# Optimization experiments

Measured on AMD Instinct MI355X. Metric: run time of the kernel, lower is better.

## Reference

```python
import jax, jax.numpy as jnp
import numpy as np

B, Z, H, T = 256, 512, 1024, 512   # batch, z_size, hidden (conductor==decoder), num_tokens
L, N = 16, 16                      # num_levels, notes_per_bar


def setup_inputs() -> dict:
    key = jax.random.key(0)
    ks = jax.random.split(key, 16)
    s = 0.05  # weight init scale
    rn = lambda k, shp, sc=1.0: sc * jax.random.normal(k, shp, dtype=jnp.float32)
    return {
        "z": rn(ks[0], (B, L * N, 1, Z)),
        "dec_h0": rn(ks[1], (L, B, H)),
        "dec_c0": rn(ks[2], (L, B, H)),
        # linear_in (computed but unused by the original forward)
        "lin_in_W": rn(ks[3], (Z, Z), s), "lin_in_b": rn(ks[4], (Z,), s),
        # conductor LSTM (input Z -> hidden H), PyTorch gate order i,f,g,o
        "cond_Wih": rn(ks[5], (4 * H, Z), s), "cond_Whh": rn(ks[6], (4 * H, H), s),
        "cond_bih": rn(ks[7], (4 * H,), s), "cond_bhh": rn(ks[8], (4 * H,), s),
        # decoder LSTM (input T+H -> hidden H)
        "dec_Wih": rn(ks[9], (4 * H, T + H), s), "dec_Whh": rn(ks[10], (4 * H, H), s),
        "dec_bih": rn(ks[11], (4 * H,), s), "dec_bhh": rn(ks[12], (4 * H,), s),
        # output projection
        "out_W": rn(ks[13], (T, H), s), "out_b": rn(ks[14], (T,), s),
    }


def _lstm_cell(x, h, c, Wih, Whh, b):
    gates = x @ Wih.T + h @ Whh.T + b            # [B, 4H]
    i, f, g, o = jnp.split(gates, 4, axis=-1)
    c = jax.nn.sigmoid(f) * c + jax.nn.sigmoid(i) * jnp.tanh(g)
    h = jax.nn.sigmoid(o) * jnp.tanh(c)
    return h, c


def reference(z, dec_h0, dec_c0, lin_in_W, lin_in_b,
              cond_Wih, cond_Whh, cond_bih, cond_bhh,
              dec_Wih, dec_Whh, dec_bih, dec_bhh, out_W, out_b):
    Bsz = z.shape[0]
    Tt = out_b.shape[0]
    Hh = cond_Whh.shape[1]

    _unused = z @ lin_in_W.T + lin_in_b  # linear_in output is discarded in the source

    cond_b = cond_bih + cond_bhh
    dec_b = dec_bih + dec_bhh

    # conductor consumes z[:, L*level, 0, :] for each level
    z_lv = jnp.transpose(z[:, jnp.arange(L) * L, 0, :], (1, 0, 2))  # [L, B, Z]

    def level_step(carry, xs):
        ch, cc = carry
        zl, dh, dc = xs
        ch, cc = _lstm_cell(zl, ch, cc, cond_Wih, cond_Whh, cond_b)
        emb = ch  # [B, H], fixed conductor embedding for this bar

        def note_step(c2, _):
            note, dh2, dc2 = c2
            inp = jnp.concatenate([emb, note], axis=-1)  # [B, H+T]
            dh2, dc2 = _lstm_cell(inp, dh2, dc2, dec_Wih, dec_Whh, dec_b)
            out = jax.nn.sigmoid(dh2 @ out_W.T + out_b)  # [B, T]
            return (out, dh2, dc2), out

        note0 = jnp.zeros((Bsz, Tt), dtype=z.dtype)
        _, outs = jax.lax.scan(note_step, (note0, dh, dc), None, length=N)  # [N, B, T]
        return (ch, cc), outs

    h0 = jnp.zeros((Bsz, Hh), dtype=z.dtype)
    _, all_outs = jax.lax.scan(level_step, (h0, h0), (z_lv, dec_h0, dec_c0))  # [L, N, B, T]
    notes = jnp.transpose(all_outs, (2, 0, 1, 3)).reshape(Bsz, L * N, Tt)
    return notes
```

## Files before the change

### kernel.cpp

```cpp
#include <hip/hip_runtime.h>

typedef __bf16 bf16;
typedef __attribute__((ext_vector_type(8))) __bf16 bf16x8;
typedef __attribute__((ext_vector_type(4))) float f32x4;
typedef __attribute__((ext_vector_type(4))) unsigned short u16x4;

__device__ __forceinline__ void gload_lds16(const void* g, void* l) {
  __builtin_amdgcn_global_load_lds(
      (const __attribute__((address_space(1))) void*)g,
      (__attribute__((address_space(3))) void*)l, 16, 0, 0);
}

__device__ __forceinline__ float sigmoidf_(float x) { return 1.0f / (1.0f + expf(-x)); }

__device__ __forceinline__ float bf2f(unsigned short u) {
  union { unsigned int i; float f; } v;
  v.i = ((unsigned int)u) << 16;
  return v.f;
}
__device__ __forceinline__ unsigned short f2bfbits(float x) {
  union { bf16 b; unsigned short u; } v;
  v.b = (bf16)x;
  return v.u;
}

#define SB() __builtin_amdgcn_sched_barrier(0)
#define BAR()                          \
  do {                                 \
    SB();                              \
    __builtin_amdgcn_s_barrier();      \
    SB();                              \
  } while (0)

#define MFMA16(a, b, c) __builtin_amdgcn_mfma_f32_16x16x32_bf16(a, b, c, 0, 0, 0)

template<int MODE>
__global__ __launch_bounds__(512, 2)
void gemm8(const bf16* __restrict__ A, int lda,
           const bf16* __restrict__ Bw, int K,
           bf16* __restrict__ Cb,
           const bf16* __restrict__ X, const float* __restrict__ bias,
           float* __restrict__ cst, bf16* __restrict__ hout, int ldh) {
  extern __shared__ __align__(16) char smem_raw[];
  bf16* lsA = (bf16*)smem_raw;
  bf16* lsB = lsA + 2 * 16384;

  const int tid = threadIdx.x;
  const int lane = tid & 63;
  const int wave = tid >> 6;
  const int wm = wave >> 2, wn = wave & 3;

  const int bid = blockIdx.x;
  const int wgid = (bid & 7) * 32 + (bid >> 3);
  const int m0 = (wgid >> 4) * 256, n0 = (wgid & 15) * 256;

  const int nkt = K >> 6;

  const int srow = tid >> 3;
  const int csw = ((tid & 7) * 8) ^ ((srow & 7) << 3);
  const bf16* gA = A + (size_t)m0 * lda + csw;
  const bf16* gB = Bw + (size_t)n0 * K + csw;

  auto stageA = [&](int kt) {
    bf16* d = lsA + (kt & 1) * 16384 + tid * 8;
    const bf16* s = gA + (size_t)srow * lda + (size_t)kt * 64;
    gload_lds16(s, d);
    gload_lds16(s + (size_t)64 * lda, d + 4096);
    gload_lds16(s + (size_t)128 * lda, d + 8192);
    gload_lds16(s + (size_t)192 * lda, d + 12288);
  };
  auto stageB = [&](int kt) {
    bf16* d = lsB + (kt & 1) * 16384 + tid * 8;
    const bf16* s = gB + (size_t)srow * K + (size_t)kt * 64;
    gload_lds16(s, d);
    gload_lds16(s + (size_t)64 * K, d + 4096);
    gload_lds16(s + (size_t)128 * K, d + 8192);
    gload_lds16(s + (size_t)192 * K, d + 12288);
  };

  const int c0 = ((lane >> 4) * 8) ^ ((lane & 7) << 3);
  const int c1 = c0 ^ 32;
  const int abase = (wm * 128 + (lane & 15)) * 64;
  const int bbase = (wn * 64 + (lane & 15)) * 64;

  f32x4 acc[8][4] = {};

  stageA(0); stageB(0);
  if (nkt > 1) stageB(1);
  if (nkt > 1) asm volatile("s_waitcnt vmcnt(4)" ::: "memory");
  else         asm volatile("s_waitcnt vmcnt(0)" ::: "memory");
  BAR();

  for (int u = 0; u < nkt; ++u) {
    const int c = u & 1;
    const bf16* pA = lsA + c * 16384;
    const bf16* pB = lsB + c * 16384;
    bf16x8 avA[4], avB[4], avC[4], avD[4], bvA[4], bvB[4];

    if (u + 1 < nkt) stageA(u + 1);
#pragma unroll
    for (int f = 0; f < 4; ++f) avA[f] = *(const bf16x8*)&pA[abase + f * 1024 + c0];
#pragma unroll
    for (int g = 0; g < 4; ++g) bvA[g] = *(const bf16x8*)&pB[bbase + g * 1024 + c0];
#pragma unroll
    for (int f = 0; f < 4; ++f) avB[f] = *(const bf16x8*)&pA[abase + (f + 4) * 1024 + c0];
    BAR();
    __builtin_amdgcn_s_setprio(1);
#pragma unroll
    for (int f = 0; f < 4; ++f)
#pragma unroll
      for (int g = 0; g < 4; ++g)
        acc[f][g] = MFMA16(avA[f], bvA[g], acc[f][g]);
    __builtin_amdgcn_s_setprio(0);
    BAR();

#pragma unroll
    for (int f = 0; f < 4; ++f) avC[f] = *(const bf16x8*)&pA[abase + f * 1024 + c1];
#pragma unroll
    for (int g = 0; g < 4; ++g) bvB[g] = *(const bf16x8*)&pB[bbase + g * 1024 + c1];
    __builtin_amdgcn_s_setprio(1);
#pragma unroll
    for (int f = 0; f < 4; ++f)
#pragma unroll
      for (int g = 0; g < 4; ++g)
        acc[f + 4][g] = MFMA16(avB[f], bvA[g], acc[f + 4][g]);
    __builtin_amdgcn_s_setprio(0);
    BAR();

#pragma unroll
    for (int f = 0; f < 4; ++f) avD[f] = *(const bf16x8*)&pA[abase + (f + 4) * 1024 + c1];
    __builtin_amdgcn_s_setprio(1);
#pragma unroll
    for (int f = 0; f < 4; ++f)
#pragma unroll
      for (int g = 0; g < 4; ++g)
        acc[f][g] = MFMA16(avC[f], bvB[g], acc[f][g]);
    __builtin_amdgcn_s_setprio(0);
    BAR();

    if (u + 2 < nkt) stageB(u + 2);
    SB();
    __builtin_amdgcn_s_setprio(1);
#pragma unroll
    for (int f = 0; f < 4; ++f)
#pragma unroll
      for (int g = 0; g < 4; ++g)
        acc[f + 4][g] = MFMA16(avD[f], bvB[g], acc[f + 4][g]);
    __builtin_amdgcn_s_setprio(0);
    if (u + 2 < nkt)      asm volatile("s_waitcnt vmcnt(4)" ::: "memory");
    else if (u + 1 < nkt) asm volatile("s_waitcnt vmcnt(0)" ::: "memory");
    BAR();
  }

  const int jj = lane & 15;
  const int rb = m0 + wm * 128 + ((lane >> 4) << 2);
  const int q = (n0 >> 6) + wn;
  if constexpr (MODE == 0) {
#pragma unroll
    for (int f = 0; f < 8; ++f)
#pragma unroll
      for (int r = 0; r < 4; ++r) {
        u16x4 pk;
        pk[0] = f2bfbits(acc[f][0][r]);
        pk[1] = f2bfbits(acc[f][1][r]);
        pk[2] = f2bfbits(acc[f][2][r]);
        pk[3] = f2bfbits(acc[f][3][r]);
        *(u16x4*)&Cb[(size_t)(rb + f * 16 + r) * 4096 + q * 64 + jj * 4] = pk;
      }
  } else {
    const int j = q * 16 + jj;
    const f32x4 bq = *(const f32x4*)&bias[q * 64 + jj * 4];
#pragma unroll
    for (int f = 0; f < 8; ++f) {
#pragma unroll
      for (int r = 0; r < 4; ++r) {
        const int row = rb + f * 16 + r;
        const u16x4 xv = *(const u16x4*)&X[(size_t)row * 4096 + q * 64 + jj * 4];
        const float gi = acc[f][0][r] + bf2f(xv[0]) + bq[0];
        const float gf = acc[f][1][r] + bf2f(xv[1]) + bq[1];
        const float gg = acc[f][2][r] + bf2f(xv[2]) + bq[2];
        const float go = acc[f][3][r] + bf2f(xv[3]) + bq[3];
        const size_t ci = (size_t)row * 1024 + j;
        const float cn = sigmoidf_(gf) * cst[ci] + sigmoidf_(gi) * tanhf(gg);
        cst[ci] = cn;
        hout[(size_t)row * ldh + j] = (bf16)(sigmoidf_(go) * tanhf(cn));
      }
    }
  }
}

template<int BM, int BN, int WM, int WN, int MODE>
__global__ __launch_bounds__(WM * WN * 64)
void gemm_bt(const bf16* __restrict__ A, int lda,
             const bf16* __restrict__ Bw, int ldb,
             float* __restrict__ C, int ldc, int K,
             const float* __restrict__ outb, float* __restrict__ dout,
             bf16* __restrict__ anote, int nstep) {
  constexpr int BK = 64;
  constexpr int THREADS = WM * WN * 64;
  constexpr int SM = BM / WM, SN = BN / WN;
  constexpr int FM = SM / 16, FN = SN / 16;

  __shared__ __align__(16) bf16 lsA[BM * BK];
  __shared__ __align__(16) bf16 lsB[BN * BK];

  const int tid = threadIdx.x;
  const int lane = tid & 63;
  const int wave = tid >> 6;
  const int wm = wave / WN, wn = wave % WN;
  const int m0 = blockIdx.y * BM;
  const int n0 = blockIdx.x * BN;

  f32x4 acc[FM][FN] = {};

  const bf16* gA = A + (size_t)m0 * lda;
  const bf16* gB = Bw + (size_t)n0 * ldb;

  for (int k0 = 0; k0 < K; k0 += BK) {
#pragma unroll
    for (int i = 0; i < (BM * 8) / THREADS; ++i) {
      int idx = i * THREADS + tid;
      gload_lds16(gA + (size_t)(idx >> 3) * lda + k0 + (idx & 7) * 8, &lsA[idx * 8]);
    }
#pragma unroll
    for (int i = 0; i < (BN * 8) / THREADS; ++i) {
      int idx = i * THREADS + tid;
      gload_lds16(gB + (size_t)(idx >> 3) * ldb + k0 + (idx & 7) * 8, &lsB[idx * 8]);
    }
    __syncthreads();

#pragma unroll
    for (int kk = 0; kk < BK; kk += 32) {
      bf16x8 av[FM], bv[FN];
#pragma unroll
      for (int i = 0; i < FM; ++i)
        av[i] = *(const bf16x8*)&lsA[(wm * SM + i * 16 + (lane & 15)) * BK + kk + (lane >> 4) * 8];
#pragma unroll
      for (int j = 0; j < FN; ++j)
        bv[j] = *(const bf16x8*)&lsB[(wn * SN + j * 16 + (lane & 15)) * BK + kk + (lane >> 4) * 8];
#pragma unroll
      for (int i = 0; i < FM; ++i)
#pragma unroll
        for (int j = 0; j < FN; ++j)
          acc[i][j] = MFMA16(av[i], bv[j], acc[i][j]);
    }
    __syncthreads();
  }

#pragma unroll
  for (int i = 0; i < FM; ++i) {
#pragma unroll
    for (int j = 0; j < FN; ++j) {
      const int col = n0 + wn * SN + j * 16 + (lane & 15);
      const int rbase = m0 + wm * SM + i * 16 + ((lane >> 4) << 2);
#pragma unroll
      for (int r = 0; r < 4; ++r) {
        const int row = rbase + r;
        float v = acc[i][j][r];
        if constexpr (MODE == 0) {
          C[(size_t)row * ldc + col] = v;
        } else {
          v = sigmoidf_(v + outb[col]);
          const int l = row >> 8, b = row & 255;
          dout[((size_t)(b * 256 + l * 16 + nstep)) * 512 + col] = v;
          anote[(size_t)row * 1536 + col] = (bf16)v;
        }
      }
    }
  }
}

template<int BM, int BJ, int WM, int WJ>
__global__ __launch_bounds__(WM * WJ * 64, 2)
void gemm_cell(const bf16* __restrict__ A, int lda,
               const bf16* __restrict__ Bw,
               const bf16* __restrict__ X,
               const float* __restrict__ bias,
               float* __restrict__ cst,
               bf16* __restrict__ hout, int ldh, int K) {
  constexpr int BK = 64;
  constexpr int THREADS = WM * WJ * 64;
  constexpr int BN = BJ * 64;
  constexpr int SM = BM / WM;
  constexpr int TJ = BJ / WJ;
  constexpr int FM = SM / 16;

  __shared__ __align__(16) bf16 lsA[BM * BK];
  __shared__ __align__(16) bf16 lsB[BN * BK];

  const int tid = threadIdx.x;
  const int lane = tid & 63;
  const int wave = tid >> 6;
  const int wm = wave / WJ, wj = wave % WJ;
  const int m0 = blockIdx.y * BM;
  const int qb = blockIdx.x * BJ;

  f32x4 acc[FM][TJ][4] = {};

  const bf16* gA = A + (size_t)m0 * lda;
  const bf16* gB = Bw + (size_t)(qb * 64) * K;

  for (int k0 = 0; k0 < K; k0 += BK) {
#pragma unroll
    for (int i = 0; i < (BM * 8) / THREADS; ++i) {
      int idx = i * THREADS + tid;
      gload_lds16(gA + (size_t)(idx >> 3) * lda + k0 + (idx & 7) * 8, &lsA[idx * 8]);
    }
#pragma unroll
    for (int i = 0; i < (BN * 8) / THREADS; ++i) {
      int idx = i * THREADS + tid;
      gload_lds16(gB + (size_t)(idx >> 3) * K + k0 + (idx & 7) * 8, &lsB[idx * 8]);
    }
    __syncthreads();

#pragma unroll
    for (int kk = 0; kk < BK; kk += 32) {
      bf16x8 av[FM], bv[TJ][4];
#pragma unroll
      for (int i = 0; i < FM; ++i)
        av[i] = *(const bf16x8*)&lsA[(wm * SM + i * 16 + (lane & 15)) * BK + kk + (lane >> 4) * 8];
#pragma unroll
      for (int t = 0; t < TJ; ++t)
#pragma unroll
        for (int g = 0; g < 4; ++g)
          bv[t][g] = *(const bf16x8*)
              &lsB[((wj * TJ + t) * 64 + g * 16 + (lane & 15)) * BK + kk + (lane >> 4) * 8];
#pragma unroll
      for (int i = 0; i < FM; ++i)
#pragma unroll
        for (int t = 0; t < TJ; ++t)
#pragma unroll
          for (int g = 0; g < 4; ++g)
            acc[i][t][g] = MFMA16(av[i], bv[t][g], acc[i][t][g]);
    }
    __syncthreads();
  }

#pragma unroll
  for (int i = 0; i < FM; ++i) {
#pragma unroll
    for (int t = 0; t < TJ; ++t) {
      const int q = qb + wj * TJ + t;
      const int jj = lane & 15;
      const int j = q * 16 + jj;
      const int rbase = m0 + wm * SM + i * 16 + ((lane >> 4) << 2);
      const f32x4 bq = *(const f32x4*)&bias[q * 64 + jj * 4];
#pragma unroll
      for (int r = 0; r < 4; ++r) {
        const int row = rbase + r;
        const u16x4 xv = *(const u16x4*)&X[(size_t)row * 4096 + q * 64 + jj * 4];
        const float gi = acc[i][t][0][r] + bf2f(xv[0]) + bq[0];
        const float gf = acc[i][t][1][r] + bf2f(xv[1]) + bq[1];
        const float gg = acc[i][t][2][r] + bf2f(xv[2]) + bq[2];
        const float go = acc[i][t][3][r] + bf2f(xv[3]) + bq[3];
        const size_t ci = (size_t)row * 1024 + j;
        const float c = sigmoidf_(gf) * cst[ci] + sigmoidf_(gi) * tanhf(gg);
        cst[ci] = c;
        hout[(size_t)row * ldh + j] = (bf16)(sigmoidf_(go) * tanhf(c));
      }
    }
  }
}


__global__ void conv_f32_bf16(const float* __restrict__ src, bf16* __restrict__ dst, int n) {
  int idx = blockIdx.x * 256 + threadIdx.x;
  if (idx < n) dst[idx] = (bf16)src[idx];
}

__device__ __forceinline__ int p_src_row(int n) {
  int q = n >> 6, gate = (n >> 4) & 3, jj = n & 15;
  return gate * 1024 + q * 16 + jj;
}

__global__ void pack_w_dec(const float* __restrict__ wih, const float* __restrict__ whh,
                           bf16* __restrict__ dst) {
  int idx = blockIdx.x * 256 + threadIdx.x;
  int n = idx / 1536, c = idx - n * 1536;
  int r = p_src_row(n);
  float v = (c < 512) ? wih[(size_t)r * 1536 + 1024 + c] : whh[(size_t)r * 1024 + (c - 512)];
  dst[idx] = (bf16)v;
}

__global__ void pack_w_emb(const float* __restrict__ wih, bf16* __restrict__ dst) {
  int idx = blockIdx.x * 256 + threadIdx.x;
  int n = idx >> 10, c = idx & 1023;
  dst[idx] = (bf16)wih[(size_t)p_src_row(n) * 1536 + c];
}

__global__ void pack_w_perm(const float* __restrict__ src, bf16* __restrict__ dst, int Kw) {
  int idx = blockIdx.x * 256 + threadIdx.x;
  int n = idx / Kw, c = idx - n * Kw;
  dst[idx] = (bf16)src[(size_t)p_src_row(n) * Kw + c];
}

__global__ void pack_bias(const float* __restrict__ bih, const float* __restrict__ bhh,
                          float* __restrict__ dst) {
  int n = blockIdx.x * 256 + threadIdx.x;
  int q = n >> 6, jj = (n >> 2) & 15, g = n & 3;
  int r = g * 1024 + q * 16 + jj;
  dst[n] = bih[r] + bhh[r];
}

__global__ void pack_zb(const float* __restrict__ z, bf16* __restrict__ dst) {
  int idx = blockIdx.x * 256 + threadIdx.x;
  int m = idx >> 9, k = idx & 511;
  int l = m >> 8, b = m & 255;
  dst[idx] = (bf16)z[((size_t)b * 256 + 16 * l) * 512 + k];
}

__global__ void init_cond(float* __restrict__ cc, bf16* __restrict__ hz0) {
  int idx = blockIdx.x * 256 + threadIdx.x;
  cc[idx] = 0.f;
  hz0[idx] = (bf16)0.f;
}

__global__ void init_state(const float* __restrict__ h0, const float* __restrict__ c0,
                           bf16* __restrict__ Abuf, float* __restrict__ cdec) {
  int idx = blockIdx.x * 256 + threadIdx.x;
  int m = idx / 1536, c = idx - m * 1536;
  if (c < 512) {
    Abuf[idx] = (bf16)0.f;
  } else {
    int j = c - 512;
    size_t s = (size_t)m * 1024 + j;
    Abuf[idx] = (bf16)h0[s];
    cdec[s] = c0[s];
  }
}

extern "C" void kernel_launch(void* const* d_in, const int* in_sizes, int n_in,
                              void* d_out, int out_size, void* d_ws, size_t ws_size,
                              hipStream_t stream) {
  const float* z        = (const float*)d_in[0];
  const float* dec_h0   = (const float*)d_in[1];
  const float* dec_c0   = (const float*)d_in[2];
  const float* cond_Wih = (const float*)d_in[5];
  const float* cond_Whh = (const float*)d_in[6];
  const float* cond_bih = (const float*)d_in[7];
  const float* cond_bhh = (const float*)d_in[8];
  const float* dec_Wih  = (const float*)d_in[9];
  const float* dec_Whh  = (const float*)d_in[10];
  const float* dec_bih  = (const float*)d_in[11];
  const float* dec_bhh  = (const float*)d_in[12];
  const float* out_W    = (const float*)d_in[13];
  const float* out_b    = (const float*)d_in[14];
  float* out = (float*)d_out;

  char* ws = (char*)d_ws;
  size_t off = 0;
  auto alloc = [&](size_t bytes) {
    void* p = ws + off;
    off += (bytes + 255) & ~(size_t)255;
    return p;
  };
  bf16* E     = (bf16*)alloc(4096ull * 4096 * 2);
  bf16* Xz    = (bf16*)alloc(4096ull * 4096 * 2);
  float* cdec = (float*)alloc(4096ull * 1024 * 4);
  bf16* Abuf  = (bf16*)alloc(4096ull * 1536 * 2);
  bf16* Wd    = (bf16*)alloc(4096ull * 1536 * 2);
  bf16* We    = (bf16*)alloc(4096ull * 1024 * 2);
  bf16* Wcih  = (bf16*)alloc(4096ull * 512 * 2);
  bf16* Wchh  = (bf16*)alloc(4096ull * 1024 * 2);
  bf16* Wo    = (bf16*)alloc(512ull * 1024 * 2);
  float* cc   = (float*)alloc(256ull * 1024 * 4);
  bf16* emb   = (bf16*)alloc(4096ull * 1024 * 2);
  bf16* Zb    = (bf16*)alloc(4096ull * 512 * 2);
  bf16* hz0   = (bf16*)alloc(256ull * 1024 * 2);
  float* bdP  = (float*)alloc(4096ull * 4);
  float* bcP  = (float*)alloc(4096ull * 4);

  dim3 b256(256);

  hipFuncSetAttribute(reinterpret_cast<const void*>(&gemm8<0>),
                      hipFuncAttributeMaxDynamicSharedMemorySize, 131072);
  hipFuncSetAttribute(reinterpret_cast<const void*>(&gemm8<1>),
                      hipFuncAttributeMaxDynamicSharedMemorySize, 131072);

  pack_w_perm<<<4096 * 512 / 256, b256, 0, stream>>>(cond_Wih, Wcih, 512);
  pack_w_perm<<<4096 * 1024 / 256, b256, 0, stream>>>(cond_Whh, Wchh, 1024);
  conv_f32_bf16<<<(512 * 1024 + 255) / 256, b256, 0, stream>>>(out_W, Wo, 512 * 1024);
  pack_w_dec<<<4096 * 1536 / 256, b256, 0, stream>>>(dec_Wih, dec_Whh, Wd);
  pack_w_emb<<<4096 * 1024 / 256, b256, 0, stream>>>(dec_Wih, We);
  pack_bias<<<16, b256, 0, stream>>>(dec_bih, dec_bhh, bdP);
  pack_bias<<<16, b256, 0, stream>>>(cond_bih, cond_bhh, bcP);
  pack_zb<<<4096 * 512 / 256, b256, 0, stream>>>(z, Zb);
  init_cond<<<256 * 1024 / 256, b256, 0, stream>>>(cc, hz0);
  init_state<<<4096 * 1536 / 256, b256, 0, stream>>>(dec_h0, dec_c0, Abuf, cdec);

  gemm8<0><<<256, 512, 131072, stream>>>(Zb, 512, Wcih, 512, Xz,
                                         nullptr, nullptr, nullptr, nullptr, 0);

  for (int l = 0; l < 16; ++l) {
    const bf16* hprev = (l == 0) ? hz0 : (emb + (size_t)(l - 1) * 256 * 1024);
    gemm_cell<32, 2, 2, 2><<<dim3(32, 8), dim3(256), 0, stream>>>(
        hprev, 1024, Wchh, Xz + (size_t)l * 256 * 4096, bcP,
        cc, emb + (size_t)l * 256 * 1024, 1024, 1024);
  }

  gemm8<0><<<256, 512, 131072, stream>>>(emb, 1024, We, 1024, E,
                                         nullptr, nullptr, nullptr, nullptr, 0);

  for (int n = 0; n < 16; ++n) {
    gemm8<1><<<256, 512, 131072, stream>>>(Abuf, 1536, Wd, 1536, nullptr,
                                           E, bdP, cdec, Abuf + 512, 1536);
    gemm_bt<128, 64, 2, 2, 1><<<dim3(512 / 64, 4096 / 128), dim3(256), 0, stream>>>(
        Abuf + 512, 1536, Wo, 1024, nullptr, 0, 1024, out_b, out, Abuf, n);
  }
}
```

Before: 1.750 ms.

## Split GEMM tile staging into half-tiles interleaved across MFMA phases

Breaks the global-to-LDS staging of the A and B tiles into two 128-row halves and issues them at different points among the four MFMA phases of each k-step. The B prefetch schedule changes to one half two steps ahead and one half one step ahead, with adjusted vmcnt waits. Fragment loads are reordered to cut the number of live register vectors. The aim is to spread memory traffic more evenly and lower register pressure. The cost is more barriers and a more delicate double-buffer hazard ordering, where the LDS halves being overwritten must already be consumed.

```diff
diff --git a/kernel.cpp b/kernel.cpp
--- a/kernel.cpp
+++ b/kernel.cpp
@@ -61,21 +61,17 @@
   const bf16* gA = A + (size_t)m0 * lda + csw;
   const bf16* gB = Bw + (size_t)n0 * K + csw;
 
-  auto stageA = [&](int kt) {
-    bf16* d = lsA + (kt & 1) * 16384 + tid * 8;
-    const bf16* s = gA + (size_t)srow * lda + (size_t)kt * 64;
+  auto stageA = [&](int kt, int h) {
+    bf16* d = lsA + (kt & 1) * 16384 + h * 8192 + tid * 8;
+    const bf16* s = gA + (size_t)(h * 128 + srow) * lda + (size_t)kt * 64;
     gload_lds16(s, d);
     gload_lds16(s + (size_t)64 * lda, d + 4096);
-    gload_lds16(s + (size_t)128 * lda, d + 8192);
-    gload_lds16(s + (size_t)192 * lda, d + 12288);
   };
-  auto stageB = [&](int kt) {
-    bf16* d = lsB + (kt & 1) * 16384 + tid * 8;
-    const bf16* s = gB + (size_t)srow * K + (size_t)kt * 64;
+  auto stageB = [&](int kt, int h) {
+    bf16* d = lsB + (kt & 1) * 16384 + h * 8192 + tid * 8;
+    const bf16* s = gB + (size_t)(h * 128 + srow) * K + (size_t)kt * 64;
     gload_lds16(s, d);
     gload_lds16(s + (size_t)64 * K, d + 4096);
-    gload_lds16(s + (size_t)128 * K, d + 8192);
-    gload_lds16(s + (size_t)192 * K, d + 12288);
   };
 
   const int c0 = ((lane >> 4) * 8) ^ ((lane & 7) << 3);
@@ -85,71 +81,88 @@
 
   f32x4 acc[8][4] = {};
 
-  stageA(0); stageB(0);
-  if (nkt > 1) stageB(1);
-  if (nkt > 1) asm volatile("s_waitcnt vmcnt(4)" ::: "memory");
-  else         asm volatile("s_waitcnt vmcnt(0)" ::: "memory");
+  stageA(0, 0); stageA(0, 1); stageB(0, 0); stageB(0, 1);
+  if (nkt > 1) {
+    stageB(1, 0);
+    asm volatile("s_waitcnt vmcnt(2)" ::: "memory");
+  } else {
+    asm volatile("s_waitcnt vmcnt(0)" ::: "memory");
+  }
   BAR();
 
   for (int u = 0; u < nkt; ++u) {
-    const int c = u & 1;
-    const bf16* pA = lsA + c * 16384;
-    const bf16* pB = lsB + c * 16384;
-    bf16x8 avA[4], avB[4], avC[4], avD[4], bvA[4], bvB[4];
-
-    if (u + 1 < nkt) stageA(u + 1);
-#pragma unroll
-    for (int f = 0; f < 4; ++f) avA[f] = *(const bf16x8*)&pA[abase + f * 1024 + c0];
-#pragma unroll
-    for (int g = 0; g < 4; ++g) bvA[g] = *(const bf16x8*)&pB[bbase + g * 1024 + c0];
-#pragma unroll
-    for (int f = 0; f < 4; ++f) avB[f] = *(const bf16x8*)&pA[abase + (f + 4) * 1024 + c0];
+    const int cb = u & 1;
+    const bf16* pA = lsA + cb * 16384;
+    const bf16* pB = lsB + cb * 16384;
+    bf16x8 av[4], bv[4];
+
+#pragma unroll
+    for (int f = 0; f < 4; ++f) av[f] = *(const bf16x8*)&pA[abase + f * 1024 + c0];
+#pragma unroll
+    for (int g = 0; g < 4; ++g) bv[g] = *(const bf16x8*)&pB[bbase + g * 1024 + c0];
+    if (u + 1 < nkt) { stageA(u + 1, 0); stageB(u + 1, 1); }
     BAR();
     __builtin_amdgcn_s_setprio(1);
 #pragma unroll
     for (int f = 0; f < 4; ++f)
 #pragma unroll
       for (int g = 0; g < 4; ++g)
-        acc[f][g] = MFMA16(avA[f], bvA[g], acc[f][g]);
+        acc[f][g] = MFMA16(av[f], bv[g], acc[f][g]);
     __builtin_amdgcn_s_setprio(0);
     BAR();
 
-#pragma unroll
-    for (int f = 0; f < 4; ++f) avC[f] = *(const bf16x8*)&pA[abase + f * 1024 + c1];
-#pragma unroll
-    for (int g = 0; g < 4; ++g) bvB[g] = *(const bf16x8*)&pB[bbase + g * 1024 + c1];
+    {
+      bf16x8 a1[4];
+#pragma unroll
+      for (int f = 0; f < 4; ++f) a1[f] = *(const bf16x8*)&pA[abase + (f + 4) * 1024 + c0];
+      if (u + 1 < nkt) stageA(u + 1, 1);
+      BAR();
+      __builtin_amdgcn_s_setprio(1);
+#pragma unroll
+      for (int f = 0; f < 4; ++f)
+#pragma unroll
+        for (int g = 0; g < 4; ++g)
+          acc[f + 4][g] = MFMA16(a1[f], bv[g], acc[f + 4][g]);
+      __builtin_amdgcn_s_setprio(0);
+      BAR();
+    }
+
+#pragma unroll
+    for (int f = 0; f < 4; ++f) av[f] = *(const bf16x8*)&pA[abase + f * 1024 + c1];
+#pragma unroll
+    for (int g = 0; g < 4; ++g) bv[g] = *(const bf16x8*)&pB[bbase + g * 1024 + c1];
+    BAR();
     __builtin_amdgcn_s_setprio(1);
 #pragma unroll
     for (int f = 0; f < 4; ++f)
 #pragma unroll
       for (int g = 0; g < 4; ++g)
-        acc[f + 4][g] = MFMA16(avB[f], bvA[g], acc[f + 4][g]);
+        acc[f][g] = MFMA16(av[f], bv[g], acc[f][g]);
     __builtin_amdgcn_s_setprio(0);
     BAR();
 
-#pragma unroll
-    for (int f = 0; f < 4; ++f) avD[f] = *(const bf16x8*)&pA[abase + (f + 4) * 1024 + c1];
-    __builtin_amdgcn_s_setprio(1);
-#pragma unroll
-    for (int f = 0; f < 4; ++f)
-#pragma unroll
-      for (int g = 0; g < 4; ++g)
-        acc[f][g] = MFMA16(avC[f], bvB[g], acc[f][g]);
-    __builtin_amdgcn_s_setprio(0);
-    BAR();
-
-    if (u + 2 < nkt) stageB(u + 2);
-    SB();
-    __builtin_amdgcn_s_setprio(1);
-#pragma unroll
-    for (int f = 0; f < 4; ++f)
-#pragma unroll
-      for (int g = 0; g < 4; ++g)
-        acc[f + 4][g] = MFMA16(avD[f], bvB[g], acc[f + 4][g]);
-    __builtin_amdgcn_s_setprio(0);
-    if (u + 2 < nkt)      asm volatile("s_waitcnt vmcnt(4)" ::: "memory");
-    else if (u + 1 < nkt) asm volatile("s_waitcnt vmcnt(0)" ::: "memory");
-    BAR();
+    {
+      bf16x8 a1[4];
+#pragma unroll
+      for (int f = 0; f < 4; ++f) a1[f] = *(const bf16x8*)&pA[abase + (f + 4) * 1024 + c1];
+      if (u + 2 < nkt) {
+        stageB(u + 2, 0);
+        SB();
+        asm volatile("s_waitcnt vmcnt(2)" ::: "memory");
+      } else {
+        SB();
+        asm volatile("s_waitcnt vmcnt(0)" ::: "memory");
+      }
+      BAR();
+      __builtin_amdgcn_s_setprio(1);
+#pragma unroll
+      for (int f = 0; f < 4; ++f)
+#pragma unroll
+        for (int g = 0; g < 4; ++g)
+          acc[f + 4][g] = MFMA16(a1[f], bv[g], acc[f + 4][g]);
+      __builtin_amdgcn_s_setprio(0);
+      BAR();
+    }
   }
 
   const int jj = lane & 15;
```

Measured after the change: 1.758 ms. About the same (+0.4%).

## Switch main GEMMs to 32x32x16 MFMA with 32-wide gate interleave and ping-pong state

Applied to the files above, without the earlier changes.

Rewrites the big fused GEMM kernel to use 32x32x16 bf16 MFMA tiles on a 4x2 wave grid. It changes the weight and bias packing so each 32-column block interleaves the four LSTM gates, and replaces the conductor cell kernel with a fixed-shape variant that uses swizzled LDS. The decoder state buffer becomes double-buffered, which removes the in-place read/write hazard, and the K-loop prefetch now loads both A and B one tile ahead with a full vmcnt(0) wait. The larger MFMA shape is meant to cut LDS reads per FLOP and instruction overhead. In exchange the pipeline is shallower and two state buffers cost extra memory.

```diff
diff --git a/kernel.cpp b/kernel.cpp
--- a/kernel.cpp
+++ b/kernel.cpp
@@ -3,6 +3,7 @@
 typedef __bf16 bf16;
 typedef __attribute__((ext_vector_type(8))) __bf16 bf16x8;
 typedef __attribute__((ext_vector_type(4))) float f32x4;
+typedef __attribute__((ext_vector_type(16))) float f32x16;
 typedef __attribute__((ext_vector_type(4))) unsigned short u16x4;
 
 __device__ __forceinline__ void gload_lds16(const void* g, void* l) {
@@ -33,14 +34,15 @@
   } while (0)
 
 #define MFMA16(a, b, c) __builtin_amdgcn_mfma_f32_16x16x32_bf16(a, b, c, 0, 0, 0)
+#define MFMA32(a, b, c) __builtin_amdgcn_mfma_f32_32x32x16_bf16(a, b, c, 0, 0, 0)
 
 template<int MODE>
 __global__ __launch_bounds__(512, 2)
-void gemm8(const bf16* __restrict__ A, int lda,
-           const bf16* __restrict__ Bw, int K,
-           bf16* __restrict__ Cb,
-           const bf16* __restrict__ X, const float* __restrict__ bias,
-           float* __restrict__ cst, bf16* __restrict__ hout, int ldh) {
+void gemm32(const bf16* __restrict__ A, int lda,
+            const bf16* __restrict__ Bw, int K,
+            bf16* __restrict__ Cb,
+            const bf16* __restrict__ X, const float* __restrict__ bias,
+            float* __restrict__ cst, bf16* __restrict__ hout, int ldh) {
   extern __shared__ __align__(16) char smem_raw[];
   bf16* lsA = (bf16*)smem_raw;
   bf16* lsB = lsA + 2 * 16384;
@@ -48,7 +50,8 @@
   const int tid = threadIdx.x;
   const int lane = tid & 63;
   const int wave = tid >> 6;
-  const int wm = wave >> 2, wn = wave & 3;
+  const int wm = wave >> 1;
+  const int wn = wave & 1;
 
   const int bid = blockIdx.x;
   const int wgid = (bid & 7) * 32 + (bid >> 3);
@@ -57,7 +60,7 @@
   const int nkt = K >> 6;
 
   const int srow = tid >> 3;
-  const int csw = ((tid & 7) * 8) ^ ((srow & 7) << 3);
+  const int csw = ((tid & 7) ^ (srow & 7)) * 8;
   const bf16* gA = A + (size_t)m0 * lda + csw;
   const bf16* gB = Bw + (size_t)n0 * K + csw;
 
@@ -78,108 +81,105 @@
     gload_lds16(s + (size_t)192 * K, d + 12288);
   };
 
-  const int c0 = ((lane >> 4) * 8) ^ ((lane & 7) << 3);
-  const int c1 = c0 ^ 32;
-  const int abase = (wm * 128 + (lane & 15)) * 64;
-  const int bbase = (wn * 64 + (lane & 15)) * 64;
-
-  f32x4 acc[8][4] = {};
+  const int kh = lane >> 5;
+  const int lx = lane & 7;
+  const int co[4] = { (((0 << 1) | kh) ^ lx) * 8, (((1 << 1) | kh) ^ lx) * 8,
+                      (((2 << 1) | kh) ^ lx) * 8, (((3 << 1) | kh) ^ lx) * 8 };
+  const int abase = (wm * 64 + (lane & 31)) * 64;
+  const int bbase = (wn * 128 + (lane & 31)) * 64;
+
+  f32x16 acc[2][4] = {};
 
   stageA(0); stageB(0);
-  if (nkt > 1) stageB(1);
-  if (nkt > 1) asm volatile("s_waitcnt vmcnt(4)" ::: "memory");
-  else         asm volatile("s_waitcnt vmcnt(0)" ::: "memory");
+  asm volatile("s_waitcnt vmcnt(0)" ::: "memory");
   BAR();
 
   for (int u = 0; u < nkt; ++u) {
-    const int c = u & 1;
-    const bf16* pA = lsA + c * 16384;
-    const bf16* pB = lsB + c * 16384;
-    bf16x8 avA[4], avB[4], avC[4], avD[4], bvA[4], bvB[4];
-
-    if (u + 1 < nkt) stageA(u + 1);
-#pragma unroll
-    for (int f = 0; f < 4; ++f) avA[f] = *(const bf16x8*)&pA[abase + f * 1024 + c0];
-#pragma unroll
-    for (int g = 0; g < 4; ++g) bvA[g] = *(const bf16x8*)&pB[bbase + g * 1024 + c0];
-#pragma unroll
-    for (int f = 0; f < 4; ++f) avB[f] = *(const bf16x8*)&pA[abase + (f + 4) * 1024 + c0];
+    const bf16* pA = lsA + (u & 1) * 16384;
+    const bf16* pB = lsB + (u & 1) * 16384;
+    bf16x8 av[2][2], bv[4][2];
+
+#pragma unroll
+    for (int r = 0; r < 2; ++r)
+#pragma unroll
+      for (int s = 0; s < 2; ++s)
+        av[r][s] = *(const bf16x8*)&pA[abase + r * 2048 + co[s]];
+#pragma unroll
+    for (int g = 0; g < 4; ++g)
+#pragma unroll
+      for (int s = 0; s < 2; ++s)
+        bv[g][s] = *(const bf16x8*)&pB[bbase + g * 2048 + co[s]];
+    if (u + 1 < nkt) { stageA(u + 1); stageB(u + 1); }
     BAR();
     __builtin_amdgcn_s_setprio(1);
 #pragma unroll
-    for (int f = 0; f < 4; ++f)
-#pragma unroll
-      for (int g = 0; g < 4; ++g)
-        acc[f][g] = MFMA16(avA[f], bvA[g], acc[f][g]);
+    for (int s = 0; s < 2; ++s)
+#pragma unroll
+      for (int r = 0; r < 2; ++r)
+#pragma unroll
+        for (int g = 0; g < 4; ++g)
+          acc[r][g] = MFMA32(av[r][s], bv[g][s], acc[r][g]);
     __builtin_amdgcn_s_setprio(0);
     BAR();
 
 #pragma unroll
-    for (int f = 0; f < 4; ++f) avC[f] = *(const bf16x8*)&pA[abase + f * 1024 + c1];
-#pragma unroll
-    for (int g = 0; g < 4; ++g) bvB[g] = *(const bf16x8*)&pB[bbase + g * 1024 + c1];
+    for (int r = 0; r < 2; ++r)
+#pragma unroll
+      for (int s = 0; s < 2; ++s)
+        av[r][s] = *(const bf16x8*)&pA[abase + r * 2048 + co[s + 2]];
+#pragma unroll
+    for (int g = 0; g < 4; ++g)
+#pragma unroll
+      for (int s = 0; s < 2; ++s)
+        bv[g][s] = *(const bf16x8*)&pB[bbase + g * 2048 + co[s + 2]];
+    BAR();
     __builtin_amdgcn_s_setprio(1);
 #pragma unroll
-    for (int f = 0; f < 4; ++f)
-#pragma unroll
-      for (int g = 0; g < 4; ++g)
-        acc[f + 4][g] = MFMA16(avB[f], bvA[g], acc[f + 4][g]);
+    for (int s = 0; s < 2; ++s)
+#pragma unroll
+      for (int r = 0; r < 2; ++r)
+#pragma unroll
+        for (int g = 0; g < 4; ++g)
+          acc[r][g] = MFMA32(av[r][s], bv[g][s], acc[r][g]);
     __builtin_amdgcn_s_setprio(0);
+    if (u + 1 < nkt) {
+      SB();
+      asm volatile("s_waitcnt vmcnt(0)" ::: "memory");
+    }
     BAR();
-
-#pragma unroll
-    for (int f = 0; f < 4; ++f) avD[f] = *(const bf16x8*)&pA[abase + (f + 4) * 1024 + c1];
-    __builtin_amdgcn_s_setprio(1);
-#pragma unroll
-    for (int f = 0; f < 4; ++f)
-#pragma unroll
-      for (int g = 0; g < 4; ++g)
-        acc[f][g] = MFMA16(avC[f], bvB[g], acc[f][g]);
-    __builtin_amdgcn_s_setprio(0);
-    BAR();
-
-    if (u + 2 < nkt) stageB(u + 2);
-    SB();
-    __builtin_amdgcn_s_setprio(1);
-#pragma unroll
-    for (int f = 0; f < 4; ++f)
-#pragma unroll
-      for (int g = 0; g < 4; ++g)
-        acc[f + 4][g] = MFMA16(avD[f], bvB[g], acc[f + 4][g]);
-    __builtin_amdgcn_s_setprio(0);
-    if (u + 2 < nkt)      asm volatile("s_waitcnt vmcnt(4)" ::: "memory");
-    else if (u + 1 < nkt) asm volatile("s_waitcnt vmcnt(0)" ::: "memory");
-    BAR();
-  }
-
-  const int jj = lane & 15;
-  const int rb = m0 + wm * 128 + ((lane >> 4) << 2);
-  const int q = (n0 >> 6) + wn;
+  }
+
+  const int jj32 = lane & 31;
+  const int q32 = (n0 >> 7) + wn;
+  const int xoff = q32 * 128 + jj32 * 4;
+  const int rb = m0 + wm * 64 + ((lane >> 5) << 2);
+
   if constexpr (MODE == 0) {
 #pragma unroll
-    for (int f = 0; f < 8; ++f)
-#pragma unroll
-      for (int r = 0; r < 4; ++r) {
+    for (int r = 0; r < 2; ++r)
+#pragma unroll
+      for (int reg = 0; reg < 16; ++reg) {
+        const int row = rb + r * 32 + (reg & 3) + 8 * (reg >> 2);
         u16x4 pk;
-        pk[0] = f2bfbits(acc[f][0][r]);
-        pk[1] = f2bfbits(acc[f][1][r]);
-        pk[2] = f2bfbits(acc[f][2][r]);
-        pk[3] = f2bfbits(acc[f][3][r]);
-        *(u16x4*)&Cb[(size_t)(rb + f * 16 + r) * 4096 + q * 64 + jj * 4] = pk;
+        pk[0] = f2bfbits(acc[r][0][reg]);
+        pk[1] = f2bfbits(acc[r][1][reg]);
+        pk[2] = f2bfbits(acc[r][2][reg]);
+        pk[3] = f2bfbits(acc[r][3][reg]);
+        *(u16x4*)&Cb[(size_t)row * 4096 + xoff] = pk;
       }
   } else {
-    const int j = q * 16 + jj;
-    const f32x4 bq = *(const f32x4*)&bias[q * 64 + jj * 4];
-#pragma unroll
-    for (int f = 0; f < 8; ++f) {
-#pragma unroll
-      for (int r = 0; r < 4; ++r) {
-        const int row = rb + f * 16 + r;
-        const u16x4 xv = *(const u16x4*)&X[(size_t)row * 4096 + q * 64 + jj * 4];
-        const float gi = acc[f][0][r] + bf2f(xv[0]) + bq[0];
-        const float gf = acc[f][1][r] + bf2f(xv[1]) + bq[1];
-        const float gg = acc[f][2][r] + bf2f(xv[2]) + bq[2];
-        const float go = acc[f][3][r] + bf2f(xv[3]) + bq[3];
+    const int j = q32 * 32 + jj32;
+    const f32x4 bq = *(const f32x4*)&bias[xoff];
+#pragma unroll
+    for (int r = 0; r < 2; ++r) {
+#pragma unroll
+      for (int reg = 0; reg < 16; ++reg) {
+        const int row = rb + r * 32 + (reg & 3) + 8 * (reg >> 2);
+        const u16x4 xv = *(const u16x4*)&X[(size_t)row * 4096 + xoff];
+        const float gi = acc[r][0][reg] + bf2f(xv[0]) + bq[0];
+        const float gf = acc[r][1][reg] + bf2f(xv[1]) + bq[1];
+        const float gg = acc[r][2][reg] + bf2f(xv[2]) + bq[2];
+        const float go = acc[r][3][reg] + bf2f(xv[3]) + bq[3];
         const size_t ci = (size_t)row * 1024 + j;
         const float cn = sigmoidf_(gf) * cst[ci] + sigmoidf_(gi) * tanhf(gg);
         cst[ci] = cn;
@@ -270,94 +270,80 @@
   }
 }
 
-template<int BM, int BJ, int WM, int WJ>
-__global__ __launch_bounds__(WM * WJ * 64, 2)
-void gemm_cell(const bf16* __restrict__ A, int lda,
-               const bf16* __restrict__ Bw,
-               const bf16* __restrict__ X,
-               const float* __restrict__ bias,
-               float* __restrict__ cst,
-               bf16* __restrict__ hout, int ldh, int K) {
-  constexpr int BK = 64;
-  constexpr int THREADS = WM * WJ * 64;
-  constexpr int BN = BJ * 64;
-  constexpr int SM = BM / WM;
-  constexpr int TJ = BJ / WJ;
-  constexpr int FM = SM / 16;
-
-  __shared__ __align__(16) bf16 lsA[BM * BK];
-  __shared__ __align__(16) bf16 lsB[BN * BK];
+__global__ __launch_bounds__(256)
+void gemm_cell_c(const bf16* __restrict__ A,
+                 const bf16* __restrict__ Bw,
+                 const bf16* __restrict__ X,
+                 const float* __restrict__ bias,
+                 float* __restrict__ cst,
+                 bf16* __restrict__ hout) {
+  __shared__ __align__(16) bf16 lsA[32 * 64];
+  __shared__ __align__(16) bf16 lsB[256 * 64];
 
   const int tid = threadIdx.x;
   const int lane = tid & 63;
   const int wave = tid >> 6;
-  const int wm = wave / WJ, wj = wave % WJ;
-  const int m0 = blockIdx.y * BM;
-  const int qb = blockIdx.x * BJ;
-
-  f32x4 acc[FM][TJ][4] = {};
-
-  const bf16* gA = A + (size_t)m0 * lda;
-  const bf16* gB = Bw + (size_t)(qb * 64) * K;
-
-  for (int k0 = 0; k0 < K; k0 += BK) {
-#pragma unroll
-    for (int i = 0; i < (BM * 8) / THREADS; ++i) {
-      int idx = i * THREADS + tid;
-      gload_lds16(gA + (size_t)(idx >> 3) * lda + k0 + (idx & 7) * 8, &lsA[idx * 8]);
-    }
-#pragma unroll
-    for (int i = 0; i < (BN * 8) / THREADS; ++i) {
-      int idx = i * THREADS + tid;
-      gload_lds16(gB + (size_t)(idx >> 3) * K + k0 + (idx & 7) * 8, &lsB[idx * 8]);
+  const int wm = wave >> 1, wj = wave & 1;
+  const int m0 = blockIdx.y * 32;
+  const int nb = blockIdx.x;
+
+  const int srow = tid >> 3;
+  const int csw = ((tid & 7) ^ (srow & 7)) * 8;
+
+  f32x4 acc[8] = {};
+
+  const int lh = lane >> 4, lx = lane & 7;
+  const int sl0 = ((0 + lh) ^ lx) * 8;
+  const int sl1 = ((4 + lh) ^ lx) * 8;
+
+  for (int kt = 0; kt < 16; ++kt) {
+    {
+      const int r = tid >> 3;
+      gload_lds16(A + (size_t)(m0 + r) * 1024 + kt * 64 + csw, &lsA[tid * 8]);
+#pragma unroll
+      for (int h = 0; h < 8; ++h) {
+        const int row = h * 32 + r;
+        gload_lds16(Bw + (size_t)(nb * 256 + row) * 1024 + kt * 64 + csw,
+                    &lsB[h * 2048 + tid * 8]);
+      }
     }
     __syncthreads();
 
 #pragma unroll
-    for (int kk = 0; kk < BK; kk += 32) {
-      bf16x8 av[FM], bv[TJ][4];
-#pragma unroll
-      for (int i = 0; i < FM; ++i)
-        av[i] = *(const bf16x8*)&lsA[(wm * SM + i * 16 + (lane & 15)) * BK + kk + (lane >> 4) * 8];
-#pragma unroll
-      for (int t = 0; t < TJ; ++t)
-#pragma unroll
-        for (int g = 0; g < 4; ++g)
-          bv[t][g] = *(const bf16x8*)
-              &lsB[((wj * TJ + t) * 64 + g * 16 + (lane & 15)) * BK + kk + (lane >> 4) * 8];
-#pragma unroll
-      for (int i = 0; i < FM; ++i)
-#pragma unroll
-        for (int t = 0; t < TJ; ++t)
-#pragma unroll
-          for (int g = 0; g < 4; ++g)
-            acc[i][t][g] = MFMA16(av[i], bv[t][g], acc[i][t][g]);
+    for (int kk = 0; kk < 2; ++kk) {
+      const int sl = kk ? sl1 : sl0;
+      bf16x8 av = *(const bf16x8*)&lsA[(wm * 16 + (lane & 15)) * 64 + sl];
+#pragma unroll
+      for (int t2 = 0; t2 < 8; ++t2) {
+        const int brow = wj * 128 + (t2 >> 1) * 32 + (t2 & 1) * 16 + (lane & 15);
+        bf16x8 bv = *(const bf16x8*)&lsB[brow * 64 + sl];
+        acc[t2] = MFMA16(av, bv, acc[t2]);
+      }
     }
     __syncthreads();
   }
 
-#pragma unroll
-  for (int i = 0; i < FM; ++i) {
-#pragma unroll
-    for (int t = 0; t < TJ; ++t) {
-      const int q = qb + wj * TJ + t;
-      const int jj = lane & 15;
-      const int j = q * 16 + jj;
-      const int rbase = m0 + wm * SM + i * 16 + ((lane >> 4) << 2);
-      const f32x4 bq = *(const f32x4*)&bias[q * 64 + jj * 4];
-#pragma unroll
-      for (int r = 0; r < 4; ++r) {
-        const int row = rbase + r;
-        const u16x4 xv = *(const u16x4*)&X[(size_t)row * 4096 + q * 64 + jj * 4];
-        const float gi = acc[i][t][0][r] + bf2f(xv[0]) + bq[0];
-        const float gf = acc[i][t][1][r] + bf2f(xv[1]) + bq[1];
-        const float gg = acc[i][t][2][r] + bf2f(xv[2]) + bq[2];
-        const float go = acc[i][t][3][r] + bf2f(xv[3]) + bq[3];
-        const size_t ci = (size_t)row * 1024 + j;
-        const float c = sigmoidf_(gf) * cst[ci] + sigmoidf_(gi) * tanhf(gg);
-        cst[ci] = c;
-        hout[(size_t)row * ldh + j] = (bf16)(sigmoidf_(go) * tanhf(c));
-      }
+  const int q32g = nb * 2 + wj;
+  const int jj = lane & 15;
+  const int rbase = m0 + wm * 16 + ((lane >> 4) << 2);
+#pragma unroll
+  for (int jh = 0; jh < 2; ++jh) {
+    const int jj32 = jh * 16 + jj;
+    const int j = q32g * 32 + jj32;
+    const int xo = q32g * 128 + jj32 * 4;
+    const f32x4 bq = *(const f32x4*)&bias[xo];
+#pragma unroll
+    for (int r = 0; r < 4; ++r) {
+      const int row = rbase + r;
+      const u16x4 xv = *(const u16x4*)&X[(size_t)row * 4096 + xo];
+      const float gi = acc[0 + jh][r] + bf2f(xv[0]) + bq[0];
+      const float gf = acc[2 + jh][r] + bf2f(xv[1]) + bq[1];
+      const float gg = acc[4 + jh][r] + bf2f(xv[2]) + bq[2];
+      const float go = acc[6 + jh][r] + bf2f(xv[3]) + bq[3];
+      const size_t ci = (size_t)row * 1024 + j;
+      const float c = sigmoidf_(gf) * cst[ci] + sigmoidf_(gi) * tanhf(gg);
+      cst[ci] = c;
+      hout[(size_t)row * 1024 + j] = (bf16)(sigmoidf_(go) * tanhf(c));
     }
   }
 }
@@ -368,16 +354,16 @@
   if (idx < n) dst[idx] = (bf16)src[idx];
 }
 
-__device__ __forceinline__ int p_src_row(int n) {
-  int q = n >> 6, gate = (n >> 4) & 3, jj = n & 15;
-  return gate * 1024 + q * 16 + jj;
+__device__ __forceinline__ int p2_src_row(int n) {
+  int q32 = n >> 7, gate = (n >> 5) & 3, jj = n & 31;
+  return gate * 1024 + q32 * 32 + jj;
 }
 
 __global__ void pack_w_dec(const float* __restrict__ wih, const float* __restrict__ whh,
                            bf16* __restrict__ dst) {
   int idx = blockIdx.x * 256 + threadIdx.x;
   int n = idx / 1536, c = idx - n * 1536;
-  int r = p_src_row(n);
+  int r = p2_src_row(n);
   float v = (c < 512) ? wih[(size_t)r * 1536 + 1024 + c] : whh[(size_t)r * 1024 + (c - 512)];
   dst[idx] = (bf16)v;
 }
@@ -385,20 +371,20 @@
 __global__ void pack_w_emb(const float* __restrict__ wih, bf16* __restrict__ dst) {
   int idx = blockIdx.x * 256 + threadIdx.x;
   int n = idx >> 10, c = idx & 1023;
-  dst[idx] = (bf16)wih[(size_t)p_src_row(n) * 1536 + c];
-}
-
-__global__ void pack_w_perm(const float* __restrict__ src, bf16* __restrict__ dst, int Kw) {
+  dst[idx] = (bf16)wih[(size_t)p2_src_row(n) * 1536 + c];
+}
+
+__global__ void pack_w_p2(const float* __restrict__ src, bf16* __restrict__ dst, int Kw) {
   int idx = blockIdx.x * 256 + threadIdx.x;
   int n = idx / Kw, c = idx - n * Kw;
-  dst[idx] = (bf16)src[(size_t)p_src_row(n) * Kw + c];
+  dst[idx] = (bf16)src[(size_t)p2_src_row(n) * Kw + c];
 }
 
 __global__ void pack_bias(const float* __restrict__ bih, const float* __restrict__ bhh,
                           float* __restrict__ dst) {
   int n = blockIdx.x * 256 + threadIdx.x;
-  int q = n >> 6, jj = (n >> 2) & 15, g = n & 3;
-  int r = g * 1024 + q * 16 + jj;
+  int q32 = n >> 7, jj = (n >> 2) & 31, g = n & 3;
+  int r = g * 1024 + q32 * 32 + jj;
   dst[n] = bih[r] + bhh[r];
 }
 
@@ -457,7 +443,8 @@
   bf16* E     = (bf16*)alloc(4096ull * 4096 * 2);
   bf16* Xz    = (bf16*)alloc(4096ull * 4096 * 2);
   float* cdec = (float*)alloc(4096ull * 1024 * 4);
-  bf16* Abuf  = (bf16*)alloc(4096ull * 1536 * 2);
+  bf16* Ab0   = (bf16*)alloc(4096ull * 1536 * 2);
+  bf16* Ab1   = (bf16*)alloc(4096ull * 1536 * 2);
   bf16* Wd    = (bf16*)alloc(4096ull * 1536 * 2);
   bf16* We    = (bf16*)alloc(4096ull * 1024 * 2);
   bf16* Wcih  = (bf16*)alloc(4096ull * 512 * 2);
@@ -472,13 +459,13 @@
 
   dim3 b256(256);
 
-  hipFuncSetAttribute(reinterpret_cast<const void*>(&gemm8<0>),
+  hipFuncSetAttribute(reinterpret_cast<const void*>(&gemm32<0>),
                       hipFuncAttributeMaxDynamicSharedMemorySize, 131072);
-  hipFuncSetAttribute(reinterpret_cast<const void*>(&gemm8<1>),
+  hipFuncSetAttribute(reinterpret_cast<const void*>(&gemm32<1>),
                       hipFuncAttributeMaxDynamicSharedMemorySize, 131072);
 
-  pack_w_perm<<<4096 * 512 / 256, b256, 0, stream>>>(cond_Wih, Wcih, 512);
-  pack_w_perm<<<4096 * 1024 / 256, b256, 0, stream>>>(cond_Whh, Wchh, 1024);
+  pack_w_p2<<<4096 * 512 / 256, b256, 0, stream>>>(cond_Wih, Wcih, 512);
+  pack_w_p2<<<4096 * 1024 / 256, b256, 0, stream>>>(cond_Whh, Wchh, 1024);
   conv_f32_bf16<<<(512 * 1024 + 255) / 256, b256, 0, stream>>>(out_W, Wo, 512 * 1024);
   pack_w_dec<<<4096 * 1536 / 256, b256, 0, stream>>>(dec_Wih, dec_Whh, Wd);
   pack_w_emb<<<4096 * 1024 / 256, b256, 0, stream>>>(dec_Wih, We);
@@ -486,25 +473,27 @@
   pack_bias<<<16, b256, 0, stream>>>(cond_bih, cond_bhh, bcP);
   pack_zb<<<4096 * 512 / 256, b256, 0, stream>>>(z, Zb);
   init_cond<<<256 * 1024 / 256, b256, 0, stream>>>(cc, hz0);
-  init_state<<<4096 * 1536 / 256, b256, 0, stream>>>(dec_h0, dec_c0, Abuf, cdec);
-
-  gemm8<0><<<256, 512, 131072, stream>>>(Zb, 512, Wcih, 512, Xz,
-                                         nullptr, nullptr, nullptr, nullptr, 0);
+  init_state<<<4096 * 1536 / 256, b256, 0, stream>>>(dec_h0, dec_c0, Ab0, cdec);
+
+  gemm32<0><<<256, 512, 131072, stream>>>(Zb, 512, Wcih, 512, Xz,
+                                          nullptr, nullptr, nullptr, nullptr, 0);
 
   for (int l = 0; l < 16; ++l) {
     const bf16* hprev = (l == 0) ? hz0 : (emb + (size_t)(l - 1) * 256 * 1024);
-    gemm_cell<32, 2, 2, 2><<<dim3(32, 8), dim3(256), 0, stream>>>(
-        hprev, 1024, Wchh, Xz + (size_t)l * 256 * 4096, bcP,
-        cc, emb + (size_t)l * 256 * 1024, 1024, 1024);
-  }
-
-  gemm8<0><<<256, 512, 131072, stream>>>(emb, 1024, We, 1024, E,
-                                         nullptr, nullptr, nullptr, nullptr, 0);
+    gemm_cell_c<<<dim3(16, 8), b256, 0, stream>>>(
+        hprev, Wchh, Xz + (size_t)l * 256 * 4096, bcP, cc,
+        emb + (size_t)l * 256 * 1024);
+  }
+
+  gemm32<0><<<256, 512, 131072, stream>>>(emb, 1024, We, 1024, E,
+                                          nullptr, nullptr, nullptr, nullptr, 0);
 
   for (int n = 0; n < 16; ++n) {
-    gemm8<1><<<256, 512, 131072, stream>>>(Abuf, 1536, Wd, 1536, nullptr,
-                                           E, bdP, cdec, Abuf + 512, 1536);
+    bf16* Sc = (n & 1) ? Ab1 : Ab0;
+    bf16* Sn = (n & 1) ? Ab0 : Ab1;
+    gemm32<1><<<256, 512, 131072, stream>>>(Sc, 1536, Wd, 1536, nullptr,
+                                            E, bdP, cdec, Sn + 512, 1536);
     gemm_bt<128, 64, 2, 2, 1><<<dim3(512 / 64, 4096 / 128), dim3(256), 0, stream>>>(
-        Abuf + 512, 1536, Wo, 1024, nullptr, 0, 1024, out_b, out, Abuf, n);
-  }
-}
+        Sn + 512, 1536, Wo, 1024, nullptr, 0, 1024, out_b, out, Sn, n);
+  }
+}
```

Result: slower. 1.997 ms (+14.1%).
